# Optimization experiments

Measured on AMD Instinct MI355X. Metric: run time of the kernel, lower is better.

Reference implementation:

```python
import jax, jax.numpy as jnp
import numpy as np

B, T, W_DIM = 32, 2048, 1024
G, D = 16, 64          # num_groups, input_dim (w = G*D)
MOM = 0.9
TH = 0.5
EPS = 1e-8
TOP_K = 2


def setup_inputs() -> dict:
    key = jax.random.key(0)
    k = jax.random.split(key, 4)
    x = jax.random.normal(k[0], (B, T, W_DIM), dtype=jnp.float32)
    ema = jnp.zeros((W_DIM, W_DIM), dtype=jnp.float32)
    W1 = jax.random.normal(k[1], (G, 16, D), dtype=jnp.float32) * 0.05
    b1 = jnp.zeros((G, 16), dtype=jnp.float32)
    W2 = jax.random.normal(k[2], (G, 1, 16), dtype=jnp.float32) * 0.05
    b2 = jnp.zeros((G, 1), dtype=jnp.float32)
    return {"x": x, "ema": ema, "W1": W1, "b1": b1, "W2": W2, "b2": b2}


def _corr_over_T(x):
    # x: (B, T, w) -> per-batch Pearson corr over the T axis: (B, w, w)
    Tn = x.shape[1]
    c = x - x.mean(axis=1, keepdims=True)
    cov = jnp.einsum('btw,btv->bwv', c, c) / (Tn - 1)
    std = jnp.sqrt(jnp.sum(c * c, axis=1) / (Tn - 1))  # (B, w)
    return jnp.clip(cov / (std[:, :, None] * std[:, None, :] + EPS), -1.0, 1.0)


def reference(x, ema, W1, b1, W2, b2):
    # --- burst-masked EMA update (torch.no_grad) ---
    corr_batch = jax.lax.stop_gradient(_corr_over_T(x))  # (B, w, w)

    def step(e, c):
        mask = jnp.abs(c) > TH
        return jnp.where(mask, MOM * e + (1.0 - MOM) * c, e), None

    ema_new, _ = jax.lax.scan(step, ema, corr_batch)

    # --- split into groups: (B, T, G, D) ---
    Bn, Tn, w = x.shape
    groups = x.reshape(Bn, Tn, G, D)

    # --- per-group correlation score: mean |off-diagonal| of within-group corr ---
    cg = groups - groups.mean(axis=1, keepdims=True)
    cov_g = jnp.einsum('btgd,btge->bgde', cg, cg) / (Tn - 1)        # (B, G, D, D)
    std_g = jnp.sqrt(jnp.sum(cg * cg, axis=1) / (Tn - 1))           # (B, G, D)
    corr_g = jnp.clip(cov_g / (std_g[..., :, None] * std_g[..., None, :] + EPS), -1.0, 1.0)
    absc = jnp.abs(corr_g)
    offdiag = (absc.sum(axis=(-2, -1)) - jnp.einsum('bgdd->bg', absc)) / (D * D - D)
    correlations = offdiag.mean(axis=0)                              # (G,)

    # --- select the 2 least-correlated groups (these get gradients) ---
    _, sel = jax.lax.top_k(-correlations, TOP_K)
    sel_mask = jnp.zeros((G,), dtype=bool).at[sel].set(True)

    # --- per-group expert MLP: D -> 16 -> 1, batched over groups ---
    h = jax.nn.relu(jnp.einsum('btgd,ghd->btgh', groups, W1) + b1)   # (B, T, G, 16)
    o = (jnp.einsum('btgh,goh->btgo', h, W2) + b2)[..., 0]           # (B, T, G)

    # non-selected groups run under no_grad -> stop_gradient on their outputs
    out = jnp.where(sel_mask[None, None, :], o, jax.lax.stop_gradient(o))
    return out, correlations, ema_new
```

## Files before the change

### kernel.cpp

```cpp
#include <hip/hip_runtime.h>
#include <hip/hip_bf16.h>
#include <stdint.h>

#define B_   32
#define T_   2048
#define W_   1024
#define G_   16
#define D_   64
#define LIST_CAP 65536
#define BK   64

typedef __bf16 bf16_t;
typedef __bf16 bf16x8 __attribute__((ext_vector_type(8)));
typedef float  f32x4  __attribute__((ext_vector_type(4)));

#define WS_XT      0ull
#define WS_XT_SZ   (134217728ull)
#define WS_SUM     (WS_XT + WS_XT_SZ)
#define WS_SQ      (WS_SUM + 131072ull)
#define WS_MU      (WS_SQ  + 131072ull)
#define WS_SIG     (WS_MU  + 131072ull)
#define WS_ACCUM   (WS_SIG + 131072ull)
#define WS_LISTCNT (WS_ACCUM + 256ull)
#define WS_LIST    (WS_LISTCNT + 256ull)
#define WS_MASK    (WS_LIST + 1048576ull)
#define WS_DIAG    (WS_MASK + 4194304ull)

__global__ __launch_bounds__(256) void stats_transpose(
    const float* __restrict__ x, bf16_t* __restrict__ xT,
    float* __restrict__ sumb, float* __restrict__ sqb) {
  int b = blockIdx.z, t0 = blockIdx.x * 64, w0 = blockIdx.y * 64;
  __shared__ float tile[64][65];
  __shared__ float rs[64][17], rq[64][17];
  int tid = threadIdx.x;
  int wc = tid & 15, tr = tid >> 4;
  float4 s4 = {0.f, 0.f, 0.f, 0.f}, q4 = {0.f, 0.f, 0.f, 0.f};
  const float4* xp = (const float4*)(x + ((size_t)b * T_ + t0) * W_ + w0);
#pragma unroll
  for (int p = 0; p < 4; ++p) {
    int t = tr + 16 * p;
    float4 v = xp[(size_t)t * 256 + wc];
    s4.x += v.x; s4.y += v.y; s4.z += v.z; s4.w += v.w;
    q4.x += v.x * v.x; q4.y += v.y * v.y; q4.z += v.z * v.z; q4.w += v.w * v.w;
    tile[4 * wc + 0][t] = v.x;
    tile[4 * wc + 1][t] = v.y;
    tile[4 * wc + 2][t] = v.z;
    tile[4 * wc + 3][t] = v.w;
  }
  rs[4 * wc + 0][tr] = s4.x; rs[4 * wc + 1][tr] = s4.y;
  rs[4 * wc + 2][tr] = s4.z; rs[4 * wc + 3][tr] = s4.w;
  rq[4 * wc + 0][tr] = q4.x; rq[4 * wc + 1][tr] = q4.y;
  rq[4 * wc + 2][tr] = q4.z; rq[4 * wc + 3][tr] = q4.w;
  __syncthreads();
  if (tid < 64) {
    float s = 0.f, q = 0.f;
#pragma unroll
    for (int i = 0; i < 16; ++i) { s += rs[tid][i]; q += rq[tid][i]; }
    atomicAdd(&sumb[b * W_ + w0 + tid], s);
    atomicAdd(&sqb[b * W_ + w0 + tid], q);
  }
  int c = tid & 7, wv = tid >> 3;
#pragma unroll
  for (int p = 0; p < 2; ++p) {
    int w = wv + 32 * p;
    const float* src = &tile[w][c * 8];
    bf16x8 o;
#pragma unroll
    for (int k = 0; k < 8; ++k) o[k] = (bf16_t)src[k];
    *(bf16x8*)(xT + ((size_t)b * W_ + w0 + w) * T_ + t0 + c * 8) = o;
  }
}

__global__ void finalize_stats(const float* __restrict__ sumb,
                               const float* __restrict__ sqb,
                               float* __restrict__ mu, float* __restrict__ sig) {
  int idx = blockIdx.x * 256 + threadIdx.x;
  float s = sumb[idx], q = sqb[idx];
  float m = s * (1.0f / 2048.0f);
  float var = (q - s * m) * (1.0f / 2047.0f);
  if (var < 0.f) var = 0.f;
  mu[idx] = m;
  sig[idx] = sqrtf(var);
}

__global__ __launch_bounds__(256) void gram_kernel(
    const bf16_t* __restrict__ xT, const float* __restrict__ mu,
    const float* __restrict__ sig, unsigned int* __restrict__ mask,
    float* __restrict__ diagv, int* __restrict__ listcnt,
    int4* __restrict__ list, float* __restrict__ accum) {
  int id = blockIdx.x;
  int xcd = id & 7;
  int idx = id >> 3;
  int sub = idx / 36;
  int rt  = idx % 36;
  int b = sub * 8 + xcd;
  int r = rt, ti = 0;
  while (r >= 8 - ti) { r -= 8 - ti; ++ti; }
  int tj = ti + r;
  int i0 = ti * 128, j0 = tj * 128;

  const bf16_t* Ag = xT + ((size_t)b * W_ + i0) * T_;
  const bf16_t* Bg = xT + ((size_t)b * W_ + j0) * T_;

  __shared__ __attribute__((aligned(16))) bf16_t As[128 * BK];
  __shared__ __attribute__((aligned(16))) bf16_t Bs[128 * BK];

  int tid = threadIdx.x;
  int lane = tid & 63, wave = tid >> 6;
  int wm = wave >> 1, wn = wave & 1;

  f32x4 zero = {0.f, 0.f, 0.f, 0.f};
  f32x4 acc[4][4];
#pragma unroll
  for (int mi = 0; mi < 4; ++mi)
#pragma unroll
    for (int nj = 0; nj < 4; ++nj) acc[mi][nj] = zero;

  int arow = wm * 64 + (lane & 15);
  int brow = wn * 64 + (lane & 15);
  int q = lane >> 4;

  for (int k0 = 0; k0 < T_; k0 += BK) {
    __syncthreads();
#pragma unroll
    for (int s = 0; s < 4; ++s) {
      int c = s * 256 + tid;
      int row = c >> 3, slot = c & 7;
      int gslot = slot ^ (row & 7);
      __builtin_amdgcn_global_load_lds(
          (const __attribute__((address_space(1))) void*)(Ag + (size_t)row * T_ + k0 + gslot * 8),
          (__attribute__((address_space(3))) void*)(As + c * 8), 16, 0, 0);
      __builtin_amdgcn_global_load_lds(
          (const __attribute__((address_space(1))) void*)(Bg + (size_t)row * T_ + k0 + gslot * 8),
          (__attribute__((address_space(3))) void*)(Bs + c * 8), 16, 0, 0);
    }
    __syncthreads();

#pragma unroll
    for (int s2 = 0; s2 < 2; ++s2) {
      bf16x8 af[4], bfr[4];
#pragma unroll
      for (int mi = 0; mi < 4; ++mi) {
        int row = arow + mi * 16;
        af[mi] = *(const bf16x8*)(As + row * BK + ((s2 * 4 + q) ^ (row & 7)) * 8);
      }
#pragma unroll
      for (int nj = 0; nj < 4; ++nj) {
        int row = brow + nj * 16;
        bfr[nj] = *(const bf16x8*)(Bs + row * BK + ((s2 * 4 + q) ^ (row & 7)) * 8);
      }
#pragma unroll
      for (int mi = 0; mi < 4; ++mi)
#pragma unroll
        for (int nj = 0; nj < 4; ++nj)
          acc[mi][nj] = __builtin_amdgcn_mfma_f32_16x16x32_bf16(af[mi], bfr[nj], acc[mi][nj], 0, 0, 0);
    }
  }

  const float inv = 1.0f / 2047.0f;
  const float* mub = mu + b * W_;
  const float* sgb = sig + b * W_;
  bool diagquad = (ti == tj) && (wm == wn);
  float gsum = 0.f;

#pragma unroll
  for (int nj = 0; nj < 4; ++nj) {
    int j = j0 + wn * 64 + nj * 16 + (lane & 15);
    float muj = mub[j], sgj = sgb[j];
#pragma unroll
    for (int mi = 0; mi < 4; ++mi) {
#pragma unroll
      for (int rr = 0; rr < 4; ++rr) {
        int i = i0 + wm * 64 + mi * 16 + (lane >> 4) * 4 + rr;
        float cov = (acc[mi][nj][rr] - 2048.0f * mub[i] * muj) * inv;
        float corr = cov / (sgb[i] * sgj + 1e-8f);
        corr = fminf(1.0f, fmaxf(-1.0f, corr));
        if (diagquad && (i != j)) gsum += fabsf(corr);
        if (fabsf(corr) > 0.5f) {
          atomicOr(&mask[i * W_ + j], 1u << b);
          if (i == j) {
            diagv[b * W_ + i] = corr;
          } else {
            int p = atomicAdd(listcnt, 1);
            if (p < LIST_CAP) list[p] = make_int4(b, i, j, __float_as_int(corr));
          }
          if (ti != tj) {
            atomicOr(&mask[j * W_ + i], 1u << b);
            int p = atomicAdd(listcnt, 1);
            if (p < LIST_CAP) list[p] = make_int4(b, j, i, __float_as_int(corr));
          }
        }
      }
    }
  }
  if (diagquad) {
    for (int o = 32; o > 0; o >>= 1) gsum += __shfl_down(gsum, o);
    if (lane == 0) atomicAdd(&accum[ti * 2 + wm], gsum);
  }
}

__global__ void ema_kernel(const float* __restrict__ ema,
                           const unsigned int* __restrict__ mask,
                           const float* __restrict__ diagv,
                           const int* __restrict__ listcnt,
                           const int4* __restrict__ list,
                           float* __restrict__ emaout) {
  int idx = blockIdx.x * 256 + threadIdx.x;
  int i = idx >> 10, j = idx & 1023;
  float e = ema[idx];
  unsigned int m = mask[idx];
  if (m) {
    if (i == j) {
      for (int b = 0; b < 32; ++b)
        if ((m >> b) & 1u) e = 0.9f * e + 0.1f * diagv[b * W_ + i];
    } else {
      int cnt = *listcnt; if (cnt > LIST_CAP) cnt = LIST_CAP;
      for (int b = 0; b < 32; ++b) {
        if ((m >> b) & 1u) {
          for (int k = 0; k < cnt; ++k) {
            int4 t = list[k];
            if (t.x == b && t.y == i && t.z == j) {
              e = 0.9f * e + 0.1f * __int_as_float(t.w);
              break;
            }
          }
        }
      }
    }
  }
  emaout[idx] = e;
}

__global__ void corr_finalize(const float* __restrict__ accum, float* __restrict__ outc) {
  int g = threadIdx.x;
  if (g < 16) outc[g] = accum[g] * (1.0f / (32.0f * 4032.0f));
}

__global__ __launch_bounds__(256) void mlp_kernel(
    const float* __restrict__ x, const float* __restrict__ W1,
    const float* __restrict__ b1, const float* __restrict__ W2,
    const float* __restrict__ b2, float* __restrict__ out) {
  int b = blockIdx.y, t0 = blockIdx.x * 64, gs = blockIdx.z * 4;
  int tid = threadIdx.x;
  int gl = tid & 3, tl = tid >> 2;
  __shared__ float Wt[16 * 64 * 4];
  __shared__ float b1s[16 * 4], W2s[16 * 4], b2s[4];
  for (int l = tid; l < 4096; l += 256) {
    int g2 = l & 3, jd = l >> 2;
    Wt[l] = W1[(size_t)(gs + g2) * 1024 + jd];
  }
  if (tid < 64) {
    int g2 = tid & 3, j = tid >> 2;
    b1s[j * 4 + g2] = b1[(gs + g2) * 16 + j];
    W2s[j * 4 + g2] = W2[(gs + g2) * 16 + j];
  }
  if (tid < 4) b2s[tid] = b2[gs + tid];
  __syncthreads();

  int g = gs + gl, t = t0 + tl;
  const float4* xp = (const float4*)(x + ((size_t)b * T_ + t) * W_ + g * D_);
  float h[16];
#pragma unroll
  for (int j = 0; j < 16; ++j) h[j] = b1s[j * 4 + gl];
#pragma unroll
  for (int d4 = 0; d4 < 16; ++d4) {
    float4 xv = xp[d4];
#pragma unroll
    for (int j = 0; j < 16; ++j) {
      const float* wp = &Wt[(j * 64 + d4 * 4) * 4 + gl];
      h[j] += xv.x * wp[0] + xv.y * wp[4] + xv.z * wp[8] + xv.w * wp[12];
    }
  }
  float o = b2s[gl];
#pragma unroll
  for (int j = 0; j < 16; ++j) o += fmaxf(h[j], 0.f) * W2s[j * 4 + gl];
  out[((size_t)b * T_ + t) * 16 + g] = o;
}

extern "C" void kernel_launch(void* const* d_in, const int* in_sizes, int n_in,
                              void* d_out, int out_size, void* d_ws, size_t ws_size,
                              hipStream_t stream) {
  const float* x   = (const float*)d_in[0];
  const float* ema = (const float*)d_in[1];
  const float* W1  = (const float*)d_in[2];
  const float* b1  = (const float*)d_in[3];
  const float* W2  = (const float*)d_in[4];
  const float* b2  = (const float*)d_in[5];

  float* out    = (float*)d_out;
  float* outc   = out + 1048576;
  float* outema = outc + 16;

  char* ws = (char*)d_ws;
  bf16_t* xT        = (bf16_t*)(ws + WS_XT);
  float* sumb       = (float*)(ws + WS_SUM);
  float* sqb        = (float*)(ws + WS_SQ);
  float* mub        = (float*)(ws + WS_MU);
  float* sigb       = (float*)(ws + WS_SIG);
  float* accum      = (float*)(ws + WS_ACCUM);
  int*   listcnt    = (int*)(ws + WS_LISTCNT);
  int4*  list       = (int4*)(ws + WS_LIST);
  unsigned int* msk = (unsigned int*)(ws + WS_MASK);
  float* diagv      = (float*)(ws + WS_DIAG);

  hipMemsetAsync(ws + WS_SUM, 0, 262144, stream);
  hipMemsetAsync(ws + WS_ACCUM, 0, 512, stream);
  hipMemsetAsync(ws + WS_MASK, 0, 4194304, stream);

  stats_transpose<<<dim3(32, 16, 32), 256, 0, stream>>>(x, xT, sumb, sqb);
  finalize_stats<<<128, 256, 0, stream>>>(sumb, sqb, mub, sigb);
  gram_kernel<<<1152, 256, 0, stream>>>(xT, mub, sigb, msk, diagv, listcnt, list, accum);
  ema_kernel<<<4096, 256, 0, stream>>>(ema, msk, diagv, listcnt, list, outema);
  corr_finalize<<<1, 16, 0, stream>>>(accum, outc);
  mlp_kernel<<<dim3(32, 32, 4), 256, 0, stream>>>(x, W1, b1, W2, b2, out);
}
```

Baseline: 728.0 us.

## Double-buffer gram kernel LDS tiles and restructure MLP kernel for register reuse

The gram kernel now uses two LDS buffers per operand and issues the async global-to-LDS loads for the next K tile before computing on the current one. This removes one barrier per iteration and overlaps memory traffic with MFMA work, at the cost of doubling LDS use (64KB), which may reduce occupancy. Separately, the MLP kernel is rewritten so each wave owns one group and each thread handles 4 timesteps. Weights are read as float4 broadcasts from a [g][d][j] LDS layout, which raises arithmetic reuse per LDS load. The trade-off is strided global reads of x across rows and more registers per thread.

```diff
diff --git a/kernel.cpp b/kernel.cpp
--- a/kernel.cpp
+++ b/kernel.cpp
@@ -102,26 +102,16 @@
   const bf16_t* Ag = xT + ((size_t)b * W_ + i0) * T_;
   const bf16_t* Bg = xT + ((size_t)b * W_ + j0) * T_;
 
-  __shared__ __attribute__((aligned(16))) bf16_t As[128 * BK];
-  __shared__ __attribute__((aligned(16))) bf16_t Bs[128 * BK];
+  __shared__ __attribute__((aligned(16))) bf16_t As[2][128 * BK];
+  __shared__ __attribute__((aligned(16))) bf16_t Bs[2][128 * BK];
 
   int tid = threadIdx.x;
   int lane = tid & 63, wave = tid >> 6;
   int wm = wave >> 1, wn = wave & 1;
 
-  f32x4 zero = {0.f, 0.f, 0.f, 0.f};
-  f32x4 acc[4][4];
-#pragma unroll
-  for (int mi = 0; mi < 4; ++mi)
-#pragma unroll
-    for (int nj = 0; nj < 4; ++nj) acc[mi][nj] = zero;
-
-  int arow = wm * 64 + (lane & 15);
-  int brow = wn * 64 + (lane & 15);
-  int q = lane >> 4;
-
-  for (int k0 = 0; k0 < T_; k0 += BK) {
-    __syncthreads();
+  auto stage = [&](int buf, int k0) {
+    bf16_t* Ad = &As[buf][0];
+    bf16_t* Bd = &Bs[buf][0];
 #pragma unroll
     for (int s = 0; s < 4; ++s) {
       int c = s * 256 + tid;
@@ -129,12 +119,33 @@
       int gslot = slot ^ (row & 7);
       __builtin_amdgcn_global_load_lds(
           (const __attribute__((address_space(1))) void*)(Ag + (size_t)row * T_ + k0 + gslot * 8),
-          (__attribute__((address_space(3))) void*)(As + c * 8), 16, 0, 0);
+          (__attribute__((address_space(3))) void*)(Ad + c * 8), 16, 0, 0);
       __builtin_amdgcn_global_load_lds(
           (const __attribute__((address_space(1))) void*)(Bg + (size_t)row * T_ + k0 + gslot * 8),
-          (__attribute__((address_space(3))) void*)(Bs + c * 8), 16, 0, 0);
-    }
-    __syncthreads();
+          (__attribute__((address_space(3))) void*)(Bd + c * 8), 16, 0, 0);
+    }
+  };
+
+  f32x4 zero = {0.f, 0.f, 0.f, 0.f};
+  f32x4 acc[4][4];
+#pragma unroll
+  for (int mi = 0; mi < 4; ++mi)
+#pragma unroll
+    for (int nj = 0; nj < 4; ++nj) acc[mi][nj] = zero;
+
+  int arow = wm * 64 + (lane & 15);
+  int brow = wn * 64 + (lane & 15);
+  int q = lane >> 4;
+
+  stage(0, 0);
+  __syncthreads();
+
+  const int NT = T_ / BK;
+  for (int kt = 0; kt < NT; ++kt) {
+    int cur = kt & 1;
+    if (kt + 1 < NT) stage(cur ^ 1, (kt + 1) * BK);
+    const bf16_t* Ac = &As[cur][0];
+    const bf16_t* Bc = &Bs[cur][0];
 
 #pragma unroll
     for (int s2 = 0; s2 < 2; ++s2) {
@@ -142,12 +153,12 @@
 #pragma unroll
       for (int mi = 0; mi < 4; ++mi) {
         int row = arow + mi * 16;
-        af[mi] = *(const bf16x8*)(As + row * BK + ((s2 * 4 + q) ^ (row & 7)) * 8);
+        af[mi] = *(const bf16x8*)(Ac + row * BK + ((s2 * 4 + q) ^ (row & 7)) * 8);
       }
 #pragma unroll
       for (int nj = 0; nj < 4; ++nj) {
         int row = brow + nj * 16;
-        bfr[nj] = *(const bf16x8*)(Bs + row * BK + ((s2 * 4 + q) ^ (row & 7)) * 8);
+        bfr[nj] = *(const bf16x8*)(Bc + row * BK + ((s2 * 4 + q) ^ (row & 7)) * 8);
       }
 #pragma unroll
       for (int mi = 0; mi < 4; ++mi)
@@ -155,6 +166,7 @@
         for (int nj = 0; nj < 4; ++nj)
           acc[mi][nj] = __builtin_amdgcn_mfma_f32_16x16x32_bf16(af[mi], bfr[nj], acc[mi][nj], 0, 0, 0);
     }
+    __syncthreads();
   }
 
   const float inv = 1.0f / 2047.0f;
@@ -240,41 +252,77 @@
     const float* __restrict__ x, const float* __restrict__ W1,
     const float* __restrict__ b1, const float* __restrict__ W2,
     const float* __restrict__ b2, float* __restrict__ out) {
-  int b = blockIdx.y, t0 = blockIdx.x * 64, gs = blockIdx.z * 4;
+  int b = blockIdx.z, t0 = blockIdx.x * 256, g0 = blockIdx.y * 4;
   int tid = threadIdx.x;
-  int gl = tid & 3, tl = tid >> 2;
-  __shared__ float Wt[16 * 64 * 4];
-  __shared__ float b1s[16 * 4], W2s[16 * 4], b2s[4];
-  for (int l = tid; l < 4096; l += 256) {
-    int g2 = l & 3, jd = l >> 2;
-    Wt[l] = W1[(size_t)(gs + g2) * 1024 + jd];
+  int wv = tid >> 6, l = tid & 63;
+  int g = g0 + wv;
+
+  __shared__ float Wt[4][64][16];
+  __shared__ float b1s[4][16], W2s[4][16], b2s[4];
+
+  for (int i = tid; i < 4096; i += 256) {
+    int gl = i >> 10, r = i & 1023, d = r >> 4, j = r & 15;
+    Wt[gl][d][j] = W1[(size_t)(g0 + gl) * 1024 + j * 64 + d];
   }
   if (tid < 64) {
-    int g2 = tid & 3, j = tid >> 2;
-    b1s[j * 4 + g2] = b1[(gs + g2) * 16 + j];
-    W2s[j * 4 + g2] = W2[(gs + g2) * 16 + j];
-  }
-  if (tid < 4) b2s[tid] = b2[gs + tid];
+    int gl = tid >> 4, j = tid & 15;
+    b1s[gl][j] = b1[(g0 + gl) * 16 + j];
+    W2s[gl][j] = W2[(g0 + gl) * 16 + j];
+  }
+  if (tid < 4) b2s[tid] = b2[g0 + tid];
   __syncthreads();
 
-  int g = gs + gl, t = t0 + tl;
-  const float4* xp = (const float4*)(x + ((size_t)b * T_ + t) * W_ + g * D_);
-  float h[16];
-#pragma unroll
-  for (int j = 0; j < 16; ++j) h[j] = b1s[j * 4 + gl];
-#pragma unroll
-  for (int d4 = 0; d4 < 16; ++d4) {
-    float4 xv = xp[d4];
-#pragma unroll
-    for (int j = 0; j < 16; ++j) {
-      const float* wp = &Wt[(j * 64 + d4 * 4) * 4 + gl];
-      h[j] += xv.x * wp[0] + xv.y * wp[4] + xv.z * wp[8] + xv.w * wp[12];
-    }
-  }
-  float o = b2s[gl];
-#pragma unroll
-  for (int j = 0; j < 16; ++j) o += fmaxf(h[j], 0.f) * W2s[j * 4 + gl];
-  out[((size_t)b * T_ + t) * 16 + g] = o;
+  const float* xg = x + ((size_t)b * T_ + t0) * W_ + g * D_;
+
+  float h[4][16];
+#pragma unroll
+  for (int tt = 0; tt < 4; ++tt)
+#pragma unroll
+    for (int j = 0; j < 16; ++j) h[tt][j] = b1s[wv][j];
+
+#pragma unroll
+  for (int d8 = 0; d8 < 8; ++d8) {
+    float4 lo[4], hi[4];
+#pragma unroll
+    for (int tt = 0; tt < 4; ++tt) {
+      const float4* xr = (const float4*)(xg + (size_t)(4 * l + tt) * W_);
+      lo[tt] = xr[2 * d8];
+      hi[tt] = xr[2 * d8 + 1];
+    }
+#pragma unroll
+    for (int half = 0; half < 2; ++half) {
+#pragma unroll
+      for (int dd = 0; dd < 4; ++dd) {
+        int d = d8 * 8 + half * 4 + dd;
+        float4 w0 = *(const float4*)&Wt[wv][d][0];
+        float4 w1 = *(const float4*)&Wt[wv][d][4];
+        float4 w2 = *(const float4*)&Wt[wv][d][8];
+        float4 w3 = *(const float4*)&Wt[wv][d][12];
+#pragma unroll
+        for (int tt = 0; tt < 4; ++tt) {
+          float xs = half ? ((const float*)&hi[tt])[dd]
+                          : ((const float*)&lo[tt])[dd];
+          h[tt][0]  += xs * w0.x; h[tt][1]  += xs * w0.y;
+          h[tt][2]  += xs * w0.z; h[tt][3]  += xs * w0.w;
+          h[tt][4]  += xs * w1.x; h[tt][5]  += xs * w1.y;
+          h[tt][6]  += xs * w1.z; h[tt][7]  += xs * w1.w;
+          h[tt][8]  += xs * w2.x; h[tt][9]  += xs * w2.y;
+          h[tt][10] += xs * w2.z; h[tt][11] += xs * w2.w;
+          h[tt][12] += xs * w3.x; h[tt][13] += xs * w3.y;
+          h[tt][14] += xs * w3.z; h[tt][15] += xs * w3.w;
+        }
+      }
+    }
+  }
+
+  float* op = out + ((size_t)b * T_ + t0 + 4 * l) * 16 + g;
+#pragma unroll
+  for (int tt = 0; tt < 4; ++tt) {
+    float o = b2s[wv];
+#pragma unroll
+    for (int j = 0; j < 16; ++j) o += fmaxf(h[tt][j], 0.f) * W2s[wv][j];
+    op[tt * 16] = o;
+  }
 }
 
 extern "C" void kernel_launch(void* const* d_in, const int* in_sizes, int n_in,
@@ -312,5 +360,5 @@
   gram_kernel<<<1152, 256, 0, stream>>>(xT, mub, sigb, msk, diagv, listcnt, list, accum);
   ema_kernel<<<4096, 256, 0, stream>>>(ema, msk, diagv, listcnt, list, outema);
   corr_finalize<<<1, 16, 0, stream>>>(accum, outc);
-  mlp_kernel<<<dim3(32, 32, 4), 256, 0, stream>>>(x, W1, b1, W2, b2, out);
-}
+  mlp_kernel<<<dim3(8, 4, 32), 256, 0, stream>>>(x, W1, b1, W2, b2, out);
+}
```

Result: slower. 819.2 us (+12.5%).
